# Performance work log

Hardware: AMD Instinct MI355X
Metric: run time of the kernel (lower is better)

## Reference

```python
import jax, jax.numpy as jnp
import numpy as np

A = 14      # num abnormalities (hardcoded 14 W_Q Linears)
QD = 64     # query_dim
H = 12      # num_heads
CH = 768    # cls_hidden_dim == H * QD (required by residual add)
B = 4096    # batch


def _layernorm(x, g, b, eps=1e-5):
    m = jnp.mean(x, axis=-1, keepdims=True)
    v = jnp.mean((x - m) ** 2, axis=-1, keepdims=True)
    return (x - m) * jax.lax.rsqrt(v + eps) * g + b


def setup_inputs() -> dict:
    key = jax.random.key(0)
    ks = jax.random.split(key, 9)
    s = 0.02
    return dict(
        classification_queries=jax.random.normal(ks[0], (A, QD), dtype=jnp.float32),
        cls_token=jax.random.normal(ks[1], (B, A, CH), dtype=jnp.float32),
        WQ=jax.random.normal(ks[2], (A, QD, QD), dtype=jnp.float32) * s,  # 14 per-abnormality query projections
        bQ=jnp.zeros((A, QD), dtype=jnp.float32),
        WK=jax.random.normal(ks[3], (H, CH, QD), dtype=jnp.float32) * s,  # per-head K projections
        bK=jnp.zeros((H, QD), dtype=jnp.float32),
        WV=jax.random.normal(ks[4], (H, CH, QD), dtype=jnp.float32) * s,  # per-head V projections
        bV=jnp.zeros((H, QD), dtype=jnp.float32),
        W1=jax.random.normal(ks[5], (H * QD, CH), dtype=jnp.float32) * s,
        b1=jnp.zeros((CH,), dtype=jnp.float32),
        W2=jax.random.normal(ks[6], (CH, CH), dtype=jnp.float32) * s,
        b2=jnp.zeros((CH,), dtype=jnp.float32),
        g1=jnp.ones((CH,), dtype=jnp.float32),
        be1=jnp.zeros((CH,), dtype=jnp.float32),
        g2=jnp.ones((CH,), dtype=jnp.float32),
        be2=jnp.zeros((CH,), dtype=jnp.float32),
    )


def reference(classification_queries, cls_token, WQ, bQ, WK, bK, WV, bV,
              W1, b1, W2, b2, g1, be1, g2, be2):
    dt = cls_token.dtype
    scale = jnp.asarray(float(QD) ** 0.5, dt)
    # Per-abnormality query projection (batched over the 14 Linears): [A, QD]
    Q = jnp.einsum('ad,adq->aq', classification_queries, WQ) + bQ
    # Per-head K/V projections, batched over heads: [B, H, S, QD] with S == A == 14
    K = jnp.einsum('bsc,hcq->bhsq', cls_token, WK) + bK[None, :, None, :]
    V = jnp.einsum('bsc,hcq->bhsq', cls_token, WV) + bV[None, :, None, :]
    # Attention scores: [B, H, A, S]; Q is broadcast across batch (torch expand)
    scores = jnp.einsum('aq,bhsq->bhas', Q, K) / scale
    # NOTE: original applies softmax over dim=1 of [B, A, S] -> the query axis 'a'
    attn = jax.nn.softmax(scores, axis=2)
    # Weighted values, heads concatenated on last dim: [B, A, H*QD]
    out = jnp.einsum('bhas,bhsq->bahq', attn, V).reshape(cls_token.shape[0], A, H * QD)
    x = _layernorm(cls_token + out, g1, be1)
    ff = jnp.maximum(jnp.dot(x, W1) + b1, 0.0) @ W2 + b2
    return _layernorm(x + ff, g2, be2)
```

## Files before the change

kernel.cpp:

```cpp
#include <hip/hip_runtime.h>
#include <stdint.h>

#define B_  4096
#define A_  14
#define QD_ 64
#define H_  12
#define CH_ 768
#define M_  (B_*A_)
#define NS_ (H_*A_)
#define N1_ (CH_+NS_)

typedef float  f32x4  __attribute__((ext_vector_type(4)));
typedef short  bf16x8 __attribute__((ext_vector_type(8)));
typedef short  s16x4  __attribute__((ext_vector_type(4)));
typedef int    i32x4  __attribute__((ext_vector_type(4)));

#define GLOAD_LDS16(gp, lp) \
  __builtin_amdgcn_global_load_lds((const __attribute__((address_space(1))) void*)(gp), \
                                   (__attribute__((address_space(3))) void*)(lp), 16, 0, 0)

__device__ __forceinline__ float b2f(ushort u) {
  union { uint32_t u; float f; } c; c.u = ((uint32_t)u) << 16; return c.f;
}
__device__ __forceinline__ ushort f2b(float f) {
  union { float f; uint32_t u; } c; c.f = f;
  uint32_t u = c.u;
  return (ushort)((u + 0x7FFFu + ((u >> 16) & 1u)) >> 16);
}


__global__ void prep_q(const float* __restrict__ cq, const float* __restrict__ WQ,
                       const float* __restrict__ bQ, float* __restrict__ Qout) {
  for (int i = threadIdx.x; i < A_*QD_; i += 256) {
    int a = i >> 6, q = i & 63;
    float acc = bQ[i];
    for (int d = 0; d < 64; ++d) acc += cq[a*64 + d] * WQ[(a*64 + d)*64 + q];
    Qout[i] = acc;
  }
}

__global__ void prep_wcat(const float* __restrict__ WV, const float* __restrict__ bV,
                          const float* __restrict__ WK, const float* __restrict__ bK,
                          const float* __restrict__ Qb, ushort* __restrict__ Wcat,
                          float* __restrict__ biascat) {
  int n = blockIdx.x, t = threadIdx.x;
  if (n < CH_) {
    int h = n >> 6, q = n & 63;
    for (int c = t; c < CH_; c += 256)
      Wcat[(size_t)n*CH_ + c] = f2b(WV[((size_t)h*CH_ + c)*64 + q]);
    if (t == 0) biascat[n] = bV[n];
  } else if (n < N1_) {
    int j = n - CH_; int h = j / 14, a = j % 14;
    __shared__ float qrow[64];
    if (t < 64) qrow[t] = Qb[a*64 + t];
    __syncthreads();
    for (int c = t; c < CH_; c += 256) {
      const float* wk = WK + ((size_t)h*CH_ + c)*64;
      float acc = 0.f;
      #pragma unroll
      for (int q = 0; q < 64; ++q) acc += qrow[q] * wk[q];
      Wcat[(size_t)n*CH_ + c] = f2b(acc * 0.125f);
    }
    if (t == 0) {
      float acc = 0.f;
      for (int q = 0; q < 64; ++q) acc += qrow[q] * bK[h*64 + q];
      biascat[n] = acc * 0.125f;
    }
  } else {
    for (int c = t; c < CH_; c += 256) Wcat[(size_t)n*CH_ + c] = 0;
    if (t == 0) biascat[n] = 0.f;
  }
}

__global__ void prep_wt(const float* __restrict__ W1, const float* __restrict__ W2,
                        ushort* __restrict__ W1T, ushort* __restrict__ W2T) {
  int i = blockIdx.x;
  int n = (i < CH_) ? i : i - CH_;
  const float* W = (i < CH_) ? W1 : W2;
  ushort* O = (i < CH_) ? W1T : W2T;
  for (int k = threadIdx.x; k < CH_; k += 256)
    O[(size_t)n*CH_ + k] = f2b(W[(size_t)k*CH_ + n]);
}

__global__ void prep_cls(const float* __restrict__ cls, ushort* __restrict__ out) {
  const size_t n4 = (size_t)M_*CH_/4;
  for (size_t i = (size_t)blockIdx.x*256 + threadIdx.x; i < n4; i += (size_t)gridDim.x*256) {
    const float* p = cls + i*4;
    s16x4 o;
    o[0] = (short)f2b(p[0]); o[1] = (short)f2b(p[1]);
    o[2] = (short)f2b(p[2]); o[3] = (short)f2b(p[3]);
    *(s16x4*)(out + i*4) = o;
  }
}

template<int MODE>
__global__ __launch_bounds__(256)
void gemm_k(const ushort* __restrict__ Ap, const ushort* __restrict__ Bp,
            const float* __restrict__ bias,
            ushort* __restrict__ Cb, float* __restrict__ Sout) {
  constexpr int GX = (MODE == 0) ? 8 : 6;
  constexpr int NWG = GX * 448;
  const int tid = threadIdx.x;
  const int wave = tid >> 6, lane = tid & 63;
  const int wm = wave >> 1, wn = wave & 1;

  const int bid = blockIdx.x;
  const int tl = (bid & 7) * (NWG >> 3) + (bid >> 3);
  const int m0 = (tl / GX) * 128, n0 = (tl % GX) * 128;

  __shared__ __align__(16) ushort Asm[2][128*64];
  __shared__ __align__(16) ushort Bsm[2][128*64];

  f32x4 acc[4][4] = {};

  const int rc = lane >> 3;
  const int sc = (lane & 7) ^ rc;
  const ushort* Abase = Ap + (size_t)(m0 + rc)*CH_ + sc*8;
  const ushort* Bbase = Bp + (size_t)(n0 + rc)*CH_ + sc*8;

  #pragma unroll
  for (int ci = 0; ci < 4; ++ci) {
    const int c = wave*4 + ci;
    GLOAD_LDS16(Abase + (size_t)c*8*CH_, &Asm[0][c*512]);
    GLOAD_LDS16(Bbase + (size_t)c*8*CH_, &Bsm[0][c*512]);
  }
  __syncthreads();

  int cur = 0;
  for (int kt = 0; kt < 12; ++kt) {
    if (kt < 11) {
      const int k0n = (kt + 1) * 64;
      #pragma unroll
      for (int ci = 0; ci < 4; ++ci) {
        const int c = wave*4 + ci;
        GLOAD_LDS16(Abase + (size_t)c*8*CH_ + k0n, &Asm[cur^1][c*512]);
        GLOAD_LDS16(Bbase + (size_t)c*8*CH_ + k0n, &Bsm[cur^1][c*512]);
      }
    }
    #pragma unroll
    for (int kk = 0; kk < 2; ++kk) {
      bf16x8 af[4], bfr[4];
      #pragma unroll
      for (int f = 0; f < 4; ++f) {
        int ar = wm*64 + f*16 + (lane & 15);
        int ab = (ar*128 + kk*64 + (lane >> 4)*16) ^ ((ar & 7) << 4);
        af[f] = *(const bf16x8*)((const char*)&Asm[cur][0] + ab);
        int br = wn*64 + f*16 + (lane & 15);
        int bb = (br*128 + kk*64 + (lane >> 4)*16) ^ ((br & 7) << 4);
        bfr[f] = *(const bf16x8*)((const char*)&Bsm[cur][0] + bb);
      }
      #pragma unroll
      for (int i = 0; i < 4; ++i)
        #pragma unroll
        for (int j = 0; j < 4; ++j)
          acc[i][j] = __builtin_amdgcn_mfma_f32_16x16x32_bf16(af[i], bfr[j], acc[i][j], 0, 0, 0);
    }
    __syncthreads();
    cur ^= 1;
  }

  #pragma unroll
  for (int j = 0; j < 4; ++j) {
    const int gc = n0 + wn*64 + j*16 + (lane & 15);
    const float bv = bias[gc];
    #pragma unroll
    for (int i = 0; i < 4; ++i) {
      const int gr0 = m0 + wm*64 + i*16 + ((lane >> 4) << 2);
      #pragma unroll
      for (int r = 0; r < 4; ++r) {
        const float v = acc[i][j][r] + bv;
        const int gr = gr0 + r;
        if (MODE == 0) {
          if (gc < CH_) {
            Cb[(size_t)gr*CH_ + gc] = f2b(v);
          } else if (gc < N1_) {
            const int j2 = gc - CH_;
            const int h = j2 / 14, a = j2 % 14;
            const int b = gr / 14, s = gr % 14;
            Sout[(((size_t)b*H_ + h)*A_ + a)*A_ + s] = v;
          }
        } else if (MODE == 1) {
          Cb[(size_t)gr*CH_ + gc] = f2b(fmaxf(v, 0.f));
        } else {
          Cb[(size_t)gr*CH_ + gc] = f2b(v);
        }
      }
    }
  }
}

__global__ __launch_bounds__(256)
void attn_ln1(const float* __restrict__ Sbuf, const ushort* __restrict__ Vbuf,
              const ushort* __restrict__ clsb, const float* __restrict__ g1,
              const float* __restrict__ be1, ushort* __restrict__ xout) {
  const int b = blockIdx.x, tid = threadIdx.x;
  const int wave = tid >> 6, lane = tid & 63;
  __shared__ __align__(16) float  s_sc[H_*A_*A_];
  __shared__ __align__(16) ushort s_v[A_*CH_];

  for (int i = tid; i < H_*A_*A_; i += 256) s_sc[i] = Sbuf[(size_t)b*H_*A_*A_ + i];
  for (int i = tid; i < A_*CH_/8; i += 256)
    *(i32x4*)((char*)s_v + i*16) = *(const i32x4*)((const char*)(Vbuf + (size_t)b*A_*CH_) + i*16);
  __syncthreads();

  if (tid < H_*A_) {
    int h = tid / 14, s = tid % 14;
    float vals[14], mx = -1e30f;
    #pragma unroll
    for (int a = 0; a < 14; ++a) { float v = s_sc[(h*14 + a)*14 + s]; vals[a] = v; mx = fmaxf(mx, v); }
    float sum = 0.f;
    #pragma unroll
    for (int a = 0; a < 14; ++a) { float e = __expf(vals[a] - mx); vals[a] = e; sum += e; }
    float inv = 1.f / sum;
    #pragma unroll
    for (int a = 0; a < 14; ++a) s_sc[(h*14 + a)*14 + s] = vals[a] * inv;
  }
  __syncthreads();

  for (int a = wave; a < A_; a += 4) {
    f32x4 vr[3]; float sum = 0.f, sq = 0.f;
    #pragma unroll
    for (int j = 0; j < 3; ++j) {
      const int c = (lane + j*64) * 4;
      const int h = c >> 6;
      const float* at = &s_sc[(h*14 + a)*14];
      f32x4 acc = {};
      #pragma unroll
      for (int s = 0; s < 14; ++s) {
        float w = at[s];
        s16x4 vv = *(const s16x4*)(&s_v[s*CH_ + c]);
        acc[0] += w * b2f((ushort)vv[0]); acc[1] += w * b2f((ushort)vv[1]);
        acc[2] += w * b2f((ushort)vv[2]); acc[3] += w * b2f((ushort)vv[3]);
      }
      s16x4 cv = *(const s16x4*)(clsb + ((size_t)b*A_ + a)*CH_ + c);
      f32x4 t;
      t[0] = b2f((ushort)cv[0]) + acc[0]; t[1] = b2f((ushort)cv[1]) + acc[1];
      t[2] = b2f((ushort)cv[2]) + acc[2]; t[3] = b2f((ushort)cv[3]) + acc[3];
      vr[j] = t;
      #pragma unroll
      for (int u = 0; u < 4; ++u) { sum += t[u]; sq += t[u]*t[u]; }
    }
    #pragma unroll
    for (int off = 32; off >= 1; off >>= 1) {
      sum += __shfl_xor(sum, off, 64);
      sq  += __shfl_xor(sq,  off, 64);
    }
    float mean = sum * (1.f/768.f);
    float var  = sq * (1.f/768.f) - mean*mean;
    float rstd = rsqrtf(var + 1e-5f);
    #pragma unroll
    for (int j = 0; j < 3; ++j) {
      int c = (lane + j*64)*4;
      f32x4 gv = *(const f32x4*)(g1 + c);
      f32x4 bv = *(const f32x4*)(be1 + c);
      s16x4 pk;
      #pragma unroll
      for (int u = 0; u < 4; ++u)
        pk[u] = (short)f2b((vr[j][u] - mean)*rstd*gv[u] + bv[u]);
      *(s16x4*)(&xout[((size_t)b*A_ + a)*CH_ + c]) = pk;
    }
  }
}

__global__ __launch_bounds__(256)
void ln2_k(const ushort* __restrict__ xb, const ushort* __restrict__ yb,
           const float* __restrict__ g2, const float* __restrict__ be2,
           float* __restrict__ out) {
  const int row = blockIdx.x*4 + (threadIdx.x >> 6);
  const int lane = threadIdx.x & 63;
  const ushort* xr = xb + (size_t)row*CH_;
  const ushort* yr = yb + (size_t)row*CH_;
  float v[12]; float sum = 0.f, sq = 0.f;
  #pragma unroll
  for (int j = 0; j < 3; ++j) {
    int c = (lane + j*64)*4;
    s16x4 xv = *(const s16x4*)(xr + c);
    s16x4 yv = *(const s16x4*)(yr + c);
    #pragma unroll
    for (int u = 0; u < 4; ++u) {
      float t = b2f((ushort)xv[u]) + b2f((ushort)yv[u]);
      v[j*4 + u] = t; sum += t; sq += t*t;
    }
  }
  #pragma unroll
  for (int off = 32; off >= 1; off >>= 1) {
    sum += __shfl_xor(sum, off, 64);
    sq  += __shfl_xor(sq,  off, 64);
  }
  float mean = sum * (1.f/768.f);
  float var  = sq * (1.f/768.f) - mean*mean;
  float rstd = rsqrtf(var + 1e-5f);
  float* orow = out + (size_t)row*CH_;
  #pragma unroll
  for (int j = 0; j < 3; ++j) {
    int c = (lane + j*64)*4;
    f32x4 gv = *(const f32x4*)(g2 + c);
    f32x4 bv = *(const f32x4*)(be2 + c);
    f32x4 o;
    #pragma unroll
    for (int u = 0; u < 4; ++u) o[u] = (v[j*4+u] - mean)*rstd*gv[u] + bv[u];
    *(f32x4*)(orow + c) = o;
  }
}

extern "C" void kernel_launch(void* const* d_in, const int* in_sizes, int n_in,
                              void* d_out, int out_size, void* d_ws, size_t ws_size,
                              hipStream_t stream) {
  const float* cq  = (const float*)d_in[0];
  const float* cls = (const float*)d_in[1];
  const float* WQ  = (const float*)d_in[2];
  const float* bQ  = (const float*)d_in[3];
  const float* WK  = (const float*)d_in[4];
  const float* bK  = (const float*)d_in[5];
  const float* WV  = (const float*)d_in[6];
  const float* bV  = (const float*)d_in[7];
  const float* W1  = (const float*)d_in[8];
  const float* b1  = (const float*)d_in[9];
  const float* W2  = (const float*)d_in[10];
  const float* b2  = (const float*)d_in[11];
  const float* g1  = (const float*)d_in[12];
  const float* be1 = (const float*)d_in[13];
  const float* g2  = (const float*)d_in[14];
  const float* be2 = (const float*)d_in[15];
  float* out = (float*)d_out;

  char* ws = (char*)d_ws;
  float*  qbuf    = (float*)(ws + 0);
  float*  biascat = (float*)(ws + 4096);
  ushort* wcat    = (ushort*)(ws + 8192);
  ushort* w1t     = (ushort*)(ws + 1581056);
  ushort* w2t     = (ushort*)(ws + 2760704);
  ushort* clsbf   = (ushort*)(ws + 4194304);
  ushort* vbuf    = (ushort*)(ws + 92274688);
  float*  sbuf    = (float*)(ws + 180355072);
  ushort* ybuf    = (ushort*)(ws + 218890240);
  ushort* xbuf  = clsbf;
  ushort* h1buf = vbuf;

  prep_q   <<<1,    256, 0, stream>>>(cq, WQ, bQ, qbuf);
  prep_wcat<<<1024, 256, 0, stream>>>(WV, bV, WK, bK, qbuf, wcat, biascat);
  prep_wt  <<<1536, 256, 0, stream>>>(W1, W2, w1t, w2t);
  prep_cls <<<2048, 256, 0, stream>>>(cls, clsbf);

  gemm_k<0><<<8*448, 256, 0, stream>>>(clsbf, wcat, biascat, vbuf, sbuf);
  attn_ln1 <<<B_, 256, 0, stream>>>(sbuf, vbuf, clsbf, g1, be1, xbuf);
  gemm_k<1><<<6*448, 256, 0, stream>>>(xbuf, w1t, b1, h1buf, nullptr);
  gemm_k<2><<<6*448, 256, 0, stream>>>(h1buf, w2t, b2, ybuf, nullptr);
  ln2_k    <<<M_/4, 256, 0, stream>>>(xbuf, ybuf, g2, be2, out);
}
```

Baseline: 699.0 us.

## Enlarge GEMM tiles to 256x256 with 8 waves and explicit vmcnt pipelining

The three bf16 GEMMs move from 128x128 tiles with 4 waves to 256x256 tiles with 8 waves (512 threads). Each wave now computes a 128x64 sub-tile, which raises operand reuse from LDS and halves global loads per FLOP. The k-loop uses explicit s_waitcnt vmcnt and raw s_barrier with sched_barriers so the next tile's loads overlap the MFMA work, and it raises wave priority around the MFMA block. The costs are 128KB of LDS per block, 128 accumulator registers, far fewer blocks, and wasted padding columns in MODE 0, where N is rounded up to 1024.

```diff
diff --git a/kernel.cpp b/kernel.cpp
--- a/kernel.cpp
+++ b/kernel.cpp
@@ -94,78 +94,90 @@
 }
 
 template<int MODE>
-__global__ __launch_bounds__(256)
+__global__ __launch_bounds__(512, 2)
 void gemm_k(const ushort* __restrict__ Ap, const ushort* __restrict__ Bp,
             const float* __restrict__ bias,
             ushort* __restrict__ Cb, float* __restrict__ Sout) {
-  constexpr int GX = (MODE == 0) ? 8 : 6;
-  constexpr int NWG = GX * 448;
+  constexpr int GN  = (MODE == 0) ? 4 : 3;
+  constexpr int NWG = 224 * GN;
   const int tid = threadIdx.x;
   const int wave = tid >> 6, lane = tid & 63;
-  const int wm = wave >> 1, wn = wave & 1;
+  const int wm = wave >> 2, wn = wave & 3;
 
   const int bid = blockIdx.x;
   const int tl = (bid & 7) * (NWG >> 3) + (bid >> 3);
-  const int m0 = (tl / GX) * 128, n0 = (tl % GX) * 128;
-
-  __shared__ __align__(16) ushort Asm[2][128*64];
-  __shared__ __align__(16) ushort Bsm[2][128*64];
-
-  f32x4 acc[4][4] = {};
-
-  const int rc = lane >> 3;
-  const int sc = (lane & 7) ^ rc;
-  const ushort* Abase = Ap + (size_t)(m0 + rc)*CH_ + sc*8;
-  const ushort* Bbase = Bp + (size_t)(n0 + rc)*CH_ + sc*8;
-
-  #pragma unroll
-  for (int ci = 0; ci < 4; ++ci) {
-    const int c = wave*4 + ci;
-    GLOAD_LDS16(Abase + (size_t)c*8*CH_, &Asm[0][c*512]);
-    GLOAD_LDS16(Bbase + (size_t)c*8*CH_, &Bsm[0][c*512]);
-  }
-  __syncthreads();
-
-  int cur = 0;
+  const int m0 = (tl / GN) * 256, n0 = (tl % GN) * 256;
+
+  __shared__ __align__(16) ushort Asm[2][256*64];
+  __shared__ __align__(16) ushort Bsm[2][256*64];
+
+  f32x4 acc[8][4] = {};
+
+  const int tq = tid >> 3;
+  const int gsc = (tid & 7) ^ (tq & 7);
+  const ushort* Ab = Ap + (size_t)(m0 + tq)*CH_ + gsc*8;
+  const ushort* Bb = Bp + (size_t)(n0 + tq)*CH_ + gsc*8;
+
+  #define STAGE_TILE(slot, k0) do {                                         \
+    _Pragma("unroll")                                                       \
+    for (int q = 0; q < 4; ++q) {                                           \
+      GLOAD_LDS16(Ab + (size_t)q*64*CH_ + (k0), &Asm[slot][q*4096 + wave*512]); \
+      GLOAD_LDS16(Bb + (size_t)q*64*CH_ + (k0), &Bsm[slot][q*4096 + wave*512]); \
+    }                                                                       \
+  } while (0)
+
+  STAGE_TILE(0, 0);
+
   for (int kt = 0; kt < 12; ++kt) {
+    const int cur = kt & 1;
     if (kt < 11) {
-      const int k0n = (kt + 1) * 64;
-      #pragma unroll
-      for (int ci = 0; ci < 4; ++ci) {
-        const int c = wave*4 + ci;
-        GLOAD_LDS16(Abase + (size_t)c*8*CH_ + k0n, &Asm[cur^1][c*512]);
-        GLOAD_LDS16(Bbase + (size_t)c*8*CH_ + k0n, &Bsm[cur^1][c*512]);
+      STAGE_TILE(cur ^ 1, (kt + 1) * 64);
+      asm volatile("s_waitcnt vmcnt(8)" ::: "memory");
+    } else {
+      asm volatile("s_waitcnt vmcnt(0)" ::: "memory");
+    }
+    __builtin_amdgcn_sched_barrier(0);
+    __builtin_amdgcn_s_barrier();
+    __builtin_amdgcn_sched_barrier(0);
+
+    const ushort* As = &Asm[cur][0];
+    const ushort* Bs = &Bsm[cur][0];
+    #pragma unroll
+    for (int kk = 0; kk < 2; ++kk) {
+      bf16x8 af[8], bfr[4];
+      #pragma unroll
+      for (int i = 0; i < 8; ++i) {
+        int ar = wm*128 + i*16 + (lane & 15);
+        int ab = (ar*128 + kk*64 + (lane >> 4)*16) ^ ((ar & 7) << 4);
+        af[i] = *(const bf16x8*)((const char*)As + ab);
       }
-    }
-    #pragma unroll
-    for (int kk = 0; kk < 2; ++kk) {
-      bf16x8 af[4], bfr[4];
-      #pragma unroll
-      for (int f = 0; f < 4; ++f) {
-        int ar = wm*64 + f*16 + (lane & 15);
-        int ab = (ar*128 + kk*64 + (lane >> 4)*16) ^ ((ar & 7) << 4);
-        af[f] = *(const bf16x8*)((const char*)&Asm[cur][0] + ab);
-        int br = wn*64 + f*16 + (lane & 15);
+      #pragma unroll
+      for (int j = 0; j < 4; ++j) {
+        int br = wn*64 + j*16 + (lane & 15);
         int bb = (br*128 + kk*64 + (lane >> 4)*16) ^ ((br & 7) << 4);
-        bfr[f] = *(const bf16x8*)((const char*)&Bsm[cur][0] + bb);
+        bfr[j] = *(const bf16x8*)((const char*)Bs + bb);
       }
-      #pragma unroll
-      for (int i = 0; i < 4; ++i)
+      __builtin_amdgcn_s_setprio(1);
+      #pragma unroll
+      for (int i = 0; i < 8; ++i)
         #pragma unroll
         for (int j = 0; j < 4; ++j)
           acc[i][j] = __builtin_amdgcn_mfma_f32_16x16x32_bf16(af[i], bfr[j], acc[i][j], 0, 0, 0);
-    }
-    __syncthreads();
-    cur ^= 1;
-  }
+      __builtin_amdgcn_s_setprio(0);
+    }
+    __builtin_amdgcn_sched_barrier(0);
+    __builtin_amdgcn_s_barrier();
+    __builtin_amdgcn_sched_barrier(0);
+  }
+  #undef STAGE_TILE
 
   #pragma unroll
   for (int j = 0; j < 4; ++j) {
     const int gc = n0 + wn*64 + j*16 + (lane & 15);
-    const float bv = bias[gc];
-    #pragma unroll
-    for (int i = 0; i < 4; ++i) {
-      const int gr0 = m0 + wm*64 + i*16 + ((lane >> 4) << 2);
+    const float bv = (MODE == 0 && gc >= N1_) ? 0.f : bias[gc];
+    #pragma unroll
+    for (int i = 0; i < 8; ++i) {
+      const int gr0 = m0 + wm*128 + i*16 + ((lane >> 4) << 2);
       #pragma unroll
       for (int r = 0; r < 4; ++r) {
         const float v = acc[i][j][r] + bv;
@@ -342,9 +354,9 @@
   prep_wt  <<<1536, 256, 0, stream>>>(W1, W2, w1t, w2t);
   prep_cls <<<2048, 256, 0, stream>>>(cls, clsbf);
 
-  gemm_k<0><<<8*448, 256, 0, stream>>>(clsbf, wcat, biascat, vbuf, sbuf);
+  gemm_k<0><<<224*4, 512, 0, stream>>>(clsbf, wcat, biascat, vbuf, sbuf);
   attn_ln1 <<<B_, 256, 0, stream>>>(sbuf, vbuf, clsbf, g1, be1, xbuf);
-  gemm_k<1><<<6*448, 256, 0, stream>>>(xbuf, w1t, b1, h1buf, nullptr);
-  gemm_k<2><<<6*448, 256, 0, stream>>>(h1buf, w2t, b2, ybuf, nullptr);
+  gemm_k<1><<<224*3, 512, 0, stream>>>(xbuf, w1t, b1, h1buf, nullptr);
+  gemm_k<2><<<224*3, 512, 0, stream>>>(h1buf, w2t, b2, ybuf, nullptr);
   ln2_k    <<<M_/4, 256, 0, stream>>>(xbuf, ybuf, g2, be2, out);
 }
```

Measured after the change: 740.4 us. +5.9%, slower.
